# Optimization experiments

Hardware: AMD Instinct MI355X
Metric: run time of the kernel (lower is better)

## Reference

```python
import jax, jax.numpy as jnp
import numpy as np

NUM_STEPS = 8
N_ETYPES = 4
N_GRAPHS = 64


def setup_inputs() -> dict:
    key = jax.random.key(0)
    ks = jax.random.split(key, 16)
    N, E, D = 50000, 500000, 128
    features = jax.random.normal(ks[0], (N, D), dtype=jnp.float32)
    src = jax.random.randint(ks[1], (E,), 0, N, dtype=jnp.int32)
    dst = jax.random.randint(ks[2], (E,), 0, N, dtype=jnp.int32)
    edge_types = jax.random.randint(ks[3], (E,), 0, N_ETYPES, dtype=jnp.int32)
    graph_ids = jnp.sort(jax.random.randint(ks[4], (N,), 0, N_GRAPHS, dtype=jnp.int32))
    s = 1.0 / np.sqrt(D)
    # per-edge-type Linear(out,out): W[t] has shape [out,in], applied as x @ W.T + b
    W_etype = jax.random.uniform(ks[5], (N_ETYPES, D, D), jnp.float32, -s, s)
    b_etype = jax.random.uniform(ks[6], (N_ETYPES, D), jnp.float32, -s, s)
    # torch GRUCell(D, D) params
    W_ih = jax.random.uniform(ks[7], (3 * D, D), jnp.float32, -s, s)
    W_hh = jax.random.uniform(ks[8], (3 * D, D), jnp.float32, -s, s)
    b_ih = jax.random.uniform(ks[9], (3 * D,), jnp.float32, -s, s)
    b_hh = jax.random.uniform(ks[10], (3 * D,), jnp.float32, -s, s)
    cls_w = jax.random.uniform(ks[11], (1, D), jnp.float32, -s, s)
    cls_b = jax.random.uniform(ks[12], (1,), jnp.float32, -s, s)
    return dict(features=features, src=src, dst=dst, edge_types=edge_types,
                graph_ids=graph_ids, W_etype=W_etype, b_etype=b_etype,
                W_ih=W_ih, W_hh=W_hh, b_ih=b_ih, b_hh=b_hh,
                cls_w=cls_w, cls_b=cls_b)


def reference(features, src, dst, edge_types, graph_ids,
              W_etype, b_etype, W_ih, W_hh, b_ih, b_hh, cls_w, cls_b):
    N = features.shape[0]

    def step(h, _):
        # transform every node's state under every edge-type linear: [T, N, D]
        T = jnp.einsum('nd,tod->tno', h, W_etype) + b_etype[:, None, :]
        msg = T[edge_types, src]                      # [E, D] gather per edge
        a = jax.ops.segment_sum(msg, dst, num_segments=N)  # scatter-sum to dst
        # torch GRUCell
        gi = a @ W_ih.T + b_ih
        gh = h @ W_hh.T + b_hh
        i_r, i_z, i_n = jnp.split(gi, 3, axis=-1)
        h_r, h_z, h_n = jnp.split(gh, 3, axis=-1)
        r = jax.nn.sigmoid(i_r + h_r)
        z = jax.nn.sigmoid(i_z + h_z)
        n = jnp.tanh(i_n + r * h_n)
        h_new = (1.0 - z) * n + z * h
        return h_new, None

    h, _ = jax.lax.scan(step, features, None, length=NUM_STEPS)
    graph_sum = jax.ops.segment_sum(h, graph_ids, num_segments=N_GRAPHS)  # [B, D]
    logits = graph_sum @ cls_w.T + cls_b                                   # [B, 1]
    return jax.nn.sigmoid(logits).squeeze(-1)                              # [B]
```

## Files before the change

### kernel.cpp

```cpp
#include <hip/hip_runtime.h>

typedef __attribute__((ext_vector_type(4))) float floatx4;
typedef __attribute__((ext_vector_type(8))) _Float16 half8;

union H2 { unsigned int u; _Float16 h[2]; };

__device__ __forceinline__ float hs2f(unsigned short u) {
    union { unsigned short u; _Float16 h; } c; c.u = u; return (float)c.h;
}
__device__ __forceinline__ unsigned short f2hs(float f) {
    union { unsigned short u; _Float16 h; } c; c.h = (_Float16)f; return c.u;
}
__device__ __forceinline__ unsigned int pack2h(float a, float b) {
    H2 c; c.h[0] = (_Float16)a; c.h[1] = (_Float16)b; return c.u;
}

__device__ __forceinline__ void load_lds16(const unsigned short* g, unsigned short* l) {
    __builtin_amdgcn_global_load_lds(
        (__attribute__((address_space(1))) void*)(g),
        (__attribute__((address_space(3))) void*)(l), 16, 0, 0);
}

__global__ void k_hist(const int* __restrict__ dst, const int* __restrict__ et,
                       int* __restrict__ cnt4, int E) {
    int i = blockIdx.x * 256 + threadIdx.x;
    if (i < E) {
        atomicAdd(&cnt4[dst[i] * 4 + et[i]], 1);
    }
}

__global__ void k_scan_blk(const int* __restrict__ cnt4, int* __restrict__ row_ptr,
                           int* __restrict__ bsum, int N) {
    __shared__ int sm[256];
    int b = blockIdx.x, t = threadIdx.x, i = b * 256 + t;
    int v = 0;
    if (i < N) {
        const int4 q = ((const int4*)cnt4)[i];
        v = q.x + q.y + q.z + q.w;
    }
    sm[t] = v;
    __syncthreads();
    for (int off = 1; off < 256; off <<= 1) {
        int x = (t >= off) ? sm[t - off] : 0;
        __syncthreads();
        sm[t] += x;
        __syncthreads();
    }
    if (i < N) row_ptr[i] = sm[t] - v;
    if (t == 255) bsum[b] = sm[255];
}

__global__ void k_scan_top(int* __restrict__ bsum, int* __restrict__ boff,
                           int* __restrict__ row_ptr, int nblocks, int N) {
    __shared__ int sm[256];
    int t = threadIdx.x;
    int v = (t < nblocks) ? bsum[t] : 0;
    sm[t] = v;
    __syncthreads();
    for (int off = 1; off < 256; off <<= 1) {
        int x = (t >= off) ? sm[t - off] : 0;
        __syncthreads();
        sm[t] += x;
        __syncthreads();
    }
    if (t < nblocks) boff[t] = sm[t] - v;
    if (t == 255) row_ptr[N] = sm[255];
}

__global__ void k_scan_add(int* __restrict__ row_ptr, int* __restrict__ cursor4,
                           const int* __restrict__ boff, const int* __restrict__ cnt4, int N) {
    int i = blockIdx.x * 256 + threadIdx.x;
    if (i < N) {
        int r = row_ptr[i] + boff[blockIdx.x];
        row_ptr[i] = r;
        const int4 q = ((const int4*)cnt4)[i];
        int4 c;
        c.x = r;
        c.y = r + q.x;
        c.z = r + q.x + q.y;
        c.w = r + q.x + q.y + q.z;
        ((int4*)cursor4)[i] = c;
    }
}

__global__ void k_scatter(const int* __restrict__ src, const int* __restrict__ dst,
                          const int* __restrict__ et, int* __restrict__ cursor4,
                          int* __restrict__ edge_pk, int E) {
    int i = blockIdx.x * 256 + threadIdx.x;
    if (i < E) {
        int p = atomicAdd(&cursor4[dst[i] * 4 + et[i]], 1);
        edge_pk[p] = src[i];
    }
}

__global__ void k_init_h(const float* __restrict__ feat, unsigned short* __restrict__ AH, int N) {
    int i = blockIdx.x * 256 + threadIdx.x;
    if (i < N * 128) {
        int v = i >> 7, d = i & 127;
        AH[(size_t)v * 256 + 128 + d] = f2hs(feat[i]);
    }
}

__global__ void k_prep_wcat(const float* __restrict__ W, unsigned short* __restrict__ w) {
    int i = blockIdx.x * 256 + threadIdx.x;
    if (i < 65536) {
        int t = i >> 14, o = (i >> 7) & 127, d = i & 127;
        w[o * 512 + t * 128 + d] = f2hs(W[i]);
    }
}

__global__ void k_prep_wrz(const float* __restrict__ Wih, const float* __restrict__ Whh,
                           unsigned short* __restrict__ w) {
    int i = blockIdx.x * 256 + threadIdx.x;
    if (i < 256 * 256) {
        int j = i >> 8, k = i & 255;
        float v = (k < 128) ? Wih[j * 128 + k] : Whh[j * 128 + (k - 128)];
        w[i] = f2hs(v);
    }
}

__global__ void k_prep_wnh(const float* __restrict__ Wih, const float* __restrict__ Whh,
                           unsigned short* __restrict__ win, unsigned short* __restrict__ whn) {
    int i = blockIdx.x * 256 + threadIdx.x;
    if (i < 128 * 128) {
        int c = i >> 7, k = i & 127;
        win[i] = f2hs(Wih[(256 + c) * 128 + k]);
        whn[i] = f2hs(Whh[(256 + c) * 128 + k]);
    }
}

__global__ __launch_bounds__(256) void k_aggregate(
    const int* __restrict__ row_ptr, const int* __restrict__ cnt4,
    const int* __restrict__ edge_pk,
    const unsigned short* __restrict__ AH, unsigned short* __restrict__ S, int N)
{
    const int wv = threadIdx.x >> 6;
    const int lane = threadIdx.x & 63;
    const int v0 = blockIdx.x * 8 + wv * 2;
    if (v0 >= N) return;
    const int v1 = v0 + 1;
    const bool has1 = (v1 < N);

    const int beg0 = __builtin_amdgcn_readfirstlane(row_ptr[v0]);
    const int end0 = __builtin_amdgcn_readfirstlane(row_ptr[v0 + 1]);
    const int end1 = has1 ? __builtin_amdgcn_readfirstlane(row_ptr[v1 + 1]) : end0;
    const int4 q0 = ((const int4*)cnt4)[v0];
    const int c1 = beg0 + __builtin_amdgcn_readfirstlane(q0.x);
    const int c2 = c1 + __builtin_amdgcn_readfirstlane(q0.y);
    const int c3 = c2 + __builtin_amdgcn_readfirstlane(q0.z);
    const int c4 = end0;
    int c5 = end0, c6 = end0, c7 = end0;
    if (has1) {
        const int4 q1 = ((const int4*)cnt4)[v1];
        c5 = end0 + __builtin_amdgcn_readfirstlane(q1.x);
        c6 = c5 + __builtin_amdgcn_readfirstlane(q1.y);
        c7 = c6 + __builtin_amdgcn_readfirstlane(q1.z);
    }

    float a0x=0,a0y=0,a1x=0,a1y=0,a2x=0,a2y=0,a3x=0,a3y=0;
    float a4x=0,a4y=0,a5x=0,a5y=0,a6x=0,a6y=0,a7x=0,a7y=0;
    const unsigned short* hbase = AH + 128 + lane * 2;

    for (int e = beg0; e < end1; e += 12) {
        int sp[12];
        unsigned int hv[12];
#pragma unroll
        for (int u = 0; u < 12; ++u) {
            int idx = e + u;
            if (idx > end1 - 1) idx = end1 - 1;
            sp[u] = edge_pk[idx];
        }
#pragma unroll
        for (int u = 0; u < 12; ++u)
            hv[u] = *(const unsigned int*)(hbase + (size_t)sp[u] * 256);
#pragma unroll
        for (int u = 0; u < 12; ++u) {
            const int idx = e + u;
            if (idx < end1) {
                H2 c; c.u = hv[u];
                float x0 = (float)c.h[0];
                float x1 = (float)c.h[1];
                if (idx < c4) {
                    if (idx < c2) { if (idx < c1) { a0x+=x0; a0y+=x1; } else { a1x+=x0; a1y+=x1; } }
                    else          { if (idx < c3) { a2x+=x0; a2y+=x1; } else { a3x+=x0; a3y+=x1; } }
                } else {
                    if (idx < c6) { if (idx < c5) { a4x+=x0; a4y+=x1; } else { a5x+=x0; a5y+=x1; } }
                    else          { if (idx < c7) { a6x+=x0; a6y+=x1; } else { a7x+=x0; a7y+=x1; } }
                }
            }
        }
    }

    unsigned int* Sp0 = (unsigned int*)&S[(size_t)v0 * 512];
    Sp0[lane]       = pack2h(a0x, a0y);
    Sp0[64 + lane]  = pack2h(a1x, a1y);
    Sp0[128 + lane] = pack2h(a2x, a2y);
    Sp0[192 + lane] = pack2h(a3x, a3y);
    if (has1) {
        unsigned int* Sp1 = (unsigned int*)&S[(size_t)v1 * 512];
        Sp1[lane]       = pack2h(a4x, a4y);
        Sp1[64 + lane]  = pack2h(a5x, a5y);
        Sp1[128 + lane] = pack2h(a6x, a6y);
        Sp1[192 + lane] = pack2h(a7x, a7y);
    }
}

__global__ __launch_bounds__(256) void k_gemm0(
    const unsigned short* __restrict__ A, int M,
    const unsigned short* __restrict__ Bw,
    unsigned short* __restrict__ outAH, const int* __restrict__ cnt4,
    const float* __restrict__ b_et)
{
    __shared__ __align__(16) unsigned short As[2][64 * 32];
    __shared__ __align__(16) unsigned short Bs[2][128 * 32];
    const int tid  = threadIdx.x;
    const int lane = tid & 63;
    const int wv   = tid >> 6;
    const int wm   = (wv & 1) * 32;
    const int wn   = (wv >> 1) * 64;
    const int mBase = blockIdx.x * 64;
    const int srow = tid >> 2;
    const int sseg = (tid & 3) * 8;
    const int Ktot = 512;

    floatx4 acc[2][4];
#pragma unroll
    for (int i = 0; i < 2; ++i)
#pragma unroll
        for (int j = 0; j < 4; ++j) acc[i][j] = (floatx4){0.f, 0.f, 0.f, 0.f};

    int r0 = mBase + srow; if (r0 >= M) r0 = M - 1;

    for (int k0 = 0; k0 < Ktot; k0 += 64) {
        __syncthreads();
#pragma unroll
        for (int sub = 0; sub < 2; ++sub) {
            const int ko = k0 + sub * 32;
            load_lds16(A + (size_t)r0 * 512 + ko + sseg, &As[sub][srow * 32 + sseg]);
            const unsigned short* bw = Bw + (size_t)srow * Ktot + ko + sseg;
            load_lds16(bw,                     &Bs[sub][srow * 32 + sseg]);
            load_lds16(bw + (size_t)64 * Ktot, &Bs[sub][(srow + 64) * 32 + sseg]);
        }
        __syncthreads();
        const int kof = (lane >> 4) * 8;
        const int mr  = lane & 15;
#pragma unroll
        for (int p = 0; p < 2; ++p) {
            half8 af[2], bf[4];
#pragma unroll
            for (int i = 0; i < 2; ++i) af[i] = *(const half8*)&As[p][(wm + i * 16 + mr) * 32 + kof];
#pragma unroll
            for (int j = 0; j < 4; ++j) bf[j] = *(const half8*)&Bs[p][(wn + j * 16 + mr) * 32 + kof];
#pragma unroll
            for (int i = 0; i < 2; ++i)
#pragma unroll
                for (int j = 0; j < 4; ++j)
                    acc[i][j] = __builtin_amdgcn_mfma_f32_16x16x32_f16(af[i], bf[j], acc[i][j], 0, 0, 0);
        }
    }

    const int mr4 = (lane >> 4) * 4;
    const int nc  = lane & 15;
#pragma unroll
    for (int i = 0; i < 2; ++i) {
#pragma unroll
        for (int r = 0; r < 4; ++r) {
            int row = mBase + wm + i * 16 + mr4 + r;
            if (row < M) {
                int cx = cnt4[row * 4 + 0], cy = cnt4[row * 4 + 1];
                int cz = cnt4[row * 4 + 2], cw = cnt4[row * 4 + 3];
#pragma unroll
                for (int j = 0; j < 4; ++j) {
                    int col = wn + j * 16 + nc;
                    float val = acc[i][j][r]
                        + (float)cx * b_et[col]       + (float)cy * b_et[128 + col]
                        + (float)cz * b_et[256 + col] + (float)cw * b_et[384 + col];
                    outAH[(size_t)row * 256 + col] = f2hs(val);
                }
            }
        }
    }
}

__global__ __launch_bounds__(256) void k_gemm1(
    const unsigned short* __restrict__ A, int M,
    const unsigned short* __restrict__ Wrz,
    const unsigned short* __restrict__ Win, const unsigned short* __restrict__ Whn,
    _Float16* __restrict__ G)
{
    __shared__ __align__(16) unsigned short As[2][64 * 32];
    __shared__ __align__(16) unsigned short Bs[2][128 * 32];
    const int tid  = threadIdx.x;
    const int lane = tid & 63;
    const int wv   = tid >> 6;
    const int wm   = (wv & 1) * 32;
    const int wn   = (wv >> 1) * 64;
    const int mBase = blockIdx.x * 64;
    const int y    = blockIdx.y;
    const int srow = tid >> 2;
    const int sseg = (tid & 3) * 8;

    const unsigned short* Bw;
    int Ktot, aOff, colBase;
    if (y < 2)      { Bw = Wrz + (size_t)y * 128 * 256; Ktot = 256; aOff = 0;   colBase = y * 128; }
    else if (y == 2){ Bw = Win; Ktot = 128; aOff = 0;   colBase = 256; }
    else            { Bw = Whn; Ktot = 128; aOff = 128; colBase = 384; }

    floatx4 acc[2][4];
#pragma unroll
    for (int i = 0; i < 2; ++i)
#pragma unroll
        for (int j = 0; j < 4; ++j) acc[i][j] = (floatx4){0.f, 0.f, 0.f, 0.f};

    int r0 = mBase + srow; if (r0 >= M) r0 = M - 1;

    for (int k0 = 0; k0 < Ktot; k0 += 64) {
        __syncthreads();
#pragma unroll
        for (int sub = 0; sub < 2; ++sub) {
            const int ko = k0 + sub * 32;
            load_lds16(A + (size_t)r0 * 256 + aOff + ko + sseg, &As[sub][srow * 32 + sseg]);
            const unsigned short* bw = Bw + (size_t)srow * Ktot + ko + sseg;
            load_lds16(bw,                     &Bs[sub][srow * 32 + sseg]);
            load_lds16(bw + (size_t)64 * Ktot, &Bs[sub][(srow + 64) * 32 + sseg]);
        }
        __syncthreads();
        const int kof = (lane >> 4) * 8;
        const int mr  = lane & 15;
#pragma unroll
        for (int p = 0; p < 2; ++p) {
            half8 af[2], bf[4];
#pragma unroll
            for (int i = 0; i < 2; ++i) af[i] = *(const half8*)&As[p][(wm + i * 16 + mr) * 32 + kof];
#pragma unroll
            for (int j = 0; j < 4; ++j) bf[j] = *(const half8*)&Bs[p][(wn + j * 16 + mr) * 32 + kof];
#pragma unroll
            for (int i = 0; i < 2; ++i)
#pragma unroll
                for (int j = 0; j < 4; ++j)
                    acc[i][j] = __builtin_amdgcn_mfma_f32_16x16x32_f16(af[i], bf[j], acc[i][j], 0, 0, 0);
        }
    }

    const int mr4 = (lane >> 4) * 4;
    const int nc  = lane & 15;
#pragma unroll
    for (int i = 0; i < 2; ++i) {
#pragma unroll
        for (int r = 0; r < 4; ++r) {
            int row = mBase + wm + i * 16 + mr4 + r;
            if (row < M) {
#pragma unroll
                for (int j = 0; j < 4; ++j) {
                    int col = colBase + wn + j * 16 + nc;
                    G[(size_t)row * 512 + col] = (_Float16)acc[i][j][r];
                }
            }
        }
    }
}

__global__ void k_gru(const _Float16* __restrict__ G, unsigned short* __restrict__ AH,
                      const float* __restrict__ b_ih, const float* __restrict__ b_hh, int N) {
    int i = blockIdx.x * 256 + threadIdx.x;
    if (i >= N * 64) return;
    int v = i >> 6, j = i & 63;
    const unsigned int* g32 = (const unsigned int*)(G + (size_t)v * 512);
    H2 pr, pz, pn, ph;
    pr.u = g32[j];
    pz.u = g32[64 + j];
    pn.u = g32[128 + j];
    ph.u = g32[192 + j];
    H2 hv; hv.u = *(const unsigned int*)&AH[(size_t)v * 256 + 128 + j * 2];
    float outs[2];
#pragma unroll
    for (int q = 0; q < 2; ++q) {
        int d = j * 2 + q;
        float pre_r = (float)pr.h[q] + b_ih[d]       + b_hh[d];
        float pre_z = (float)pz.h[q] + b_ih[128 + d] + b_hh[128 + d];
        float i_n   = (float)pn.h[q] + b_ih[256 + d];
        float h_n   = (float)ph.h[q] + b_hh[256 + d];
        float r = 1.f / (1.f + __expf(-pre_r));
        float z = 1.f / (1.f + __expf(-pre_z));
        float n = tanhf(i_n + r * h_n);
        float h = (float)hv.h[q];
        outs[q] = (1.f - z) * n + z * h;
    }
    *(unsigned int*)&AH[(size_t)v * 256 + 128 + j * 2] = pack2h(outs[0], outs[1]);
}

__global__ void k_dotv(const unsigned short* __restrict__ AH, const float* __restrict__ cls_w,
                       float* __restrict__ dotv, int N) {
    int v = blockIdx.x * 4 + (threadIdx.x >> 6);
    int lane = threadIdx.x & 63;
    if (v >= N) return;
    H2 c; c.u = *(const unsigned int*)&AH[(size_t)v * 256 + 128 + lane * 2];
    float x = (float)c.h[0] * cls_w[lane * 2]
            + (float)c.h[1] * cls_w[lane * 2 + 1];
#pragma unroll
    for (int off = 32; off > 0; off >>= 1) x += __shfl_down(x, off);
    if (lane == 0) dotv[v] = x;
}

__global__ void k_gsum(const float* __restrict__ dotv, const int* __restrict__ gids,
                       const float* __restrict__ cls_b, float* __restrict__ out, int N) {
    int g = blockIdx.x;
    int t = threadIdx.x;
    int lo = 0, hi = N;
    while (lo < hi) { int m = (lo + hi) >> 1; if (gids[m] < g) lo = m + 1; else hi = m; }
    int s = lo;
    lo = 0; hi = N;
    while (lo < hi) { int m = (lo + hi) >> 1; if (gids[m] < g + 1) lo = m + 1; else hi = m; }
    int e = lo;
    float acc = 0.f;
    for (int v = s + t; v < e; v += 256) acc += dotv[v];
    __shared__ float red[256];
    red[t] = acc;
    __syncthreads();
    for (int off = 128; off > 0; off >>= 1) {
        if (t < off) red[t] += red[t + off];
        __syncthreads();
    }
    if (t == 0) out[g] = 1.f / (1.f + expf(-(red[0] + cls_b[0])));
}

extern "C" void kernel_launch(void* const* d_in, const int* in_sizes, int n_in,
                              void* d_out, int out_size, void* d_ws, size_t ws_size,
                              hipStream_t stream) {
    const float* features = (const float*)d_in[0];
    const int*   src      = (const int*)d_in[1];
    const int*   dst      = (const int*)d_in[2];
    const int*   etype    = (const int*)d_in[3];
    const int*   gids     = (const int*)d_in[4];
    const float* W_etype  = (const float*)d_in[5];
    const float* b_etype  = (const float*)d_in[6];
    const float* W_ih     = (const float*)d_in[7];
    const float* W_hh     = (const float*)d_in[8];
    const float* b_ih     = (const float*)d_in[9];
    const float* b_hh     = (const float*)d_in[10];
    const float* cls_w    = (const float*)d_in[11];
    const float* cls_b    = (const float*)d_in[12];
    const int N = in_sizes[0] / 128;
    const int E = in_sizes[1];
    float* out = (float*)d_out;

    char* ws = (char*)d_ws;
    size_t off = 0;
    auto alloc = [&](size_t bytes) -> void* {
        off = (off + 255) & ~(size_t)255;
        void* p = ws + off;
        off += bytes;
        return p;
    };
    unsigned short* AH  = (unsigned short*)alloc((size_t)N * 256 * 2);
    unsigned short* S   = (unsigned short*)alloc((size_t)N * 512 * 2);
    _Float16*       G   = (_Float16*)alloc((size_t)N * 512 * 2);
    unsigned short* Wc  = (unsigned short*)alloc(128 * 512 * 2);
    unsigned short* Wrz = (unsigned short*)alloc(256 * 256 * 2);
    unsigned short* Win = (unsigned short*)alloc(128 * 128 * 2);
    unsigned short* Whn = (unsigned short*)alloc(128 * 128 * 2);
    int* row_ptr = (int*)alloc((size_t)(N + 1) * 4);
    int* cursor4 = (int*)alloc((size_t)N * 16);
    int* cnt4    = (int*)alloc((size_t)N * 16);
    int* edge_pk = (int*)alloc((size_t)E * 4);
    float* dotv  = (float*)alloc((size_t)N * 4);
    int* bsum    = (int*)alloc(256 * 4);
    int* boff    = (int*)alloc(256 * 4);
    (void)ws_size; (void)n_in;

    const int nscan = (N + 255) / 256;
    hipMemsetAsync(cnt4, 0, (size_t)N * 16, stream);
    k_hist<<<(E + 255) / 256, 256, 0, stream>>>(dst, etype, cnt4, E);
    k_scan_blk<<<nscan, 256, 0, stream>>>(cnt4, row_ptr, bsum, N);
    k_scan_top<<<1, 256, 0, stream>>>(bsum, boff, row_ptr, nscan, N);
    k_scan_add<<<nscan, 256, 0, stream>>>(row_ptr, cursor4, boff, cnt4, N);
    k_scatter<<<(E + 255) / 256, 256, 0, stream>>>(src, dst, etype, cursor4, edge_pk, E);
    k_init_h<<<(N * 128 + 255) / 256, 256, 0, stream>>>(features, AH, N);
    k_prep_wcat<<<65536 / 256, 256, 0, stream>>>(W_etype, Wc);
    k_prep_wrz<<<(256 * 256) / 256, 256, 0, stream>>>(W_ih, W_hh, Wrz);
    k_prep_wnh<<<(128 * 128) / 256, 256, 0, stream>>>(W_ih, W_hh, Win, Whn);

    const int mblocks64 = (N + 63) / 64;
    for (int s = 0; s < 8; ++s) {
        k_aggregate<<<(N + 7) / 8, 256, 0, stream>>>(row_ptr, cnt4, edge_pk, AH, S, N);
        k_gemm0<<<mblocks64, 256, 0, stream>>>(S, N, Wc, AH, cnt4, b_etype);
        dim3 g2(mblocks64, 4);
        k_gemm1<<<g2, 256, 0, stream>>>(AH, N, Wrz, Win, Whn, G);
        k_gru<<<(N * 64 + 255) / 256, 256, 0, stream>>>(G, AH, b_ih, b_hh, N);
    }
    k_dotv<<<(N + 3) / 4, 256, 0, stream>>>(AH, cls_w, dotv, N);
    k_gsum<<<out_size, 256, 0, stream>>>(dotv, gids, cls_b, out, N);
}
```

Baseline: 958.4 us.

## Fuse GRU gate GEMMs and elementwise update into one kernel

Replaces the 4-way split gate GEMM plus a separate GRU elementwise kernel with a single kernel per 64-row tile. It computes the r/z, i_n and h_n products in sequence and applies the GRU update in the epilogue, writing h back into AH in place. This removes the N×512 fp16 G buffer round trip and one launch per step. In exchange the grid has a quarter as many blocks, register pressure is higher (r, z and n results are kept packed in registers), and the per-element epilogue stores are strided. The in-place write is safe only because each block reads just its own rows.

```diff
diff --git a/kernel.cpp b/kernel.cpp
--- a/kernel.cpp
+++ b/kernel.cpp
@@ -282,51 +282,95 @@
     }
 }
 
-__global__ __launch_bounds__(256) void k_gemm1(
-    const unsigned short* __restrict__ A, int M,
+__global__ __launch_bounds__(256) void k_gates(
+    unsigned short* AH, int M,
     const unsigned short* __restrict__ Wrz,
     const unsigned short* __restrict__ Win, const unsigned short* __restrict__ Whn,
-    _Float16* __restrict__ G)
+    const float* __restrict__ b_ih, const float* __restrict__ b_hh)
 {
     __shared__ __align__(16) unsigned short As[2][64 * 32];
-    __shared__ __align__(16) unsigned short Bs[2][128 * 32];
+    __shared__ __align__(16) unsigned short Bs[2][256 * 32];
     const int tid  = threadIdx.x;
     const int lane = tid & 63;
     const int wv   = tid >> 6;
     const int wm   = (wv & 1) * 32;
     const int wn   = (wv >> 1) * 64;
     const int mBase = blockIdx.x * 64;
-    const int y    = blockIdx.y;
     const int srow = tid >> 2;
     const int sseg = (tid & 3) * 8;
-
-    const unsigned short* Bw;
-    int Ktot, aOff, colBase;
-    if (y < 2)      { Bw = Wrz + (size_t)y * 128 * 256; Ktot = 256; aOff = 0;   colBase = y * 128; }
-    else if (y == 2){ Bw = Win; Ktot = 128; aOff = 0;   colBase = 256; }
-    else            { Bw = Whn; Ktot = 128; aOff = 128; colBase = 384; }
-
-    floatx4 acc[2][4];
+    const int kof  = (lane >> 4) * 8;
+    const int mr   = lane & 15;
+
+    int r0 = mBase + srow; if (r0 >= M) r0 = M - 1;
+
+    floatx4 acc_r[2][4], acc_z[2][4];
 #pragma unroll
     for (int i = 0; i < 2; ++i)
 #pragma unroll
-        for (int j = 0; j < 4; ++j) acc[i][j] = (floatx4){0.f, 0.f, 0.f, 0.f};
-
-    int r0 = mBase + srow; if (r0 >= M) r0 = M - 1;
-
-    for (int k0 = 0; k0 < Ktot; k0 += 64) {
+        for (int j = 0; j < 4; ++j) {
+            acc_r[i][j] = (floatx4){0.f, 0.f, 0.f, 0.f};
+            acc_z[i][j] = (floatx4){0.f, 0.f, 0.f, 0.f};
+        }
+
+    for (int k0 = 0; k0 < 256; k0 += 64) {
         __syncthreads();
 #pragma unroll
         for (int sub = 0; sub < 2; ++sub) {
             const int ko = k0 + sub * 32;
-            load_lds16(A + (size_t)r0 * 256 + aOff + ko + sseg, &As[sub][srow * 32 + sseg]);
-            const unsigned short* bw = Bw + (size_t)srow * Ktot + ko + sseg;
-            load_lds16(bw,                     &Bs[sub][srow * 32 + sseg]);
-            load_lds16(bw + (size_t)64 * Ktot, &Bs[sub][(srow + 64) * 32 + sseg]);
-        }
-        __syncthreads();
-        const int kof = (lane >> 4) * 8;
-        const int mr  = lane & 15;
+            load_lds16(AH + (size_t)r0 * 256 + ko + sseg, &As[sub][srow * 32 + sseg]);
+            const unsigned short* b = Wrz + (size_t)srow * 256 + ko + sseg;
+            load_lds16(b,                     &Bs[sub][srow * 32 + sseg]);
+            load_lds16(b + (size_t)64 * 256,  &Bs[sub][(srow + 64) * 32 + sseg]);
+            load_lds16(b + (size_t)128 * 256, &Bs[sub][(srow + 128) * 32 + sseg]);
+            load_lds16(b + (size_t)192 * 256, &Bs[sub][(srow + 192) * 32 + sseg]);
+        }
+        __syncthreads();
+#pragma unroll
+        for (int p = 0; p < 2; ++p) {
+            half8 af[2], br[4], bz[4];
+#pragma unroll
+            for (int i = 0; i < 2; ++i) af[i] = *(const half8*)&As[p][(wm + i * 16 + mr) * 32 + kof];
+#pragma unroll
+            for (int j = 0; j < 4; ++j) br[j] = *(const half8*)&Bs[p][(wn + j * 16 + mr) * 32 + kof];
+#pragma unroll
+            for (int j = 0; j < 4; ++j) bz[j] = *(const half8*)&Bs[p][(128 + wn + j * 16 + mr) * 32 + kof];
+#pragma unroll
+            for (int i = 0; i < 2; ++i)
+#pragma unroll
+                for (int j = 0; j < 4; ++j) {
+                    acc_r[i][j] = __builtin_amdgcn_mfma_f32_16x16x32_f16(af[i], br[j], acc_r[i][j], 0, 0, 0);
+                    acc_z[i][j] = __builtin_amdgcn_mfma_f32_16x16x32_f16(af[i], bz[j], acc_z[i][j], 0, 0, 0);
+                }
+        }
+    }
+    unsigned int r_pk[2][4][2], z_pk[2][4][2];
+#pragma unroll
+    for (int i = 0; i < 2; ++i)
+#pragma unroll
+        for (int j = 0; j < 4; ++j) {
+            r_pk[i][j][0] = pack2h(acc_r[i][j][0], acc_r[i][j][1]);
+            r_pk[i][j][1] = pack2h(acc_r[i][j][2], acc_r[i][j][3]);
+            z_pk[i][j][0] = pack2h(acc_z[i][j][0], acc_z[i][j][1]);
+            z_pk[i][j][1] = pack2h(acc_z[i][j][2], acc_z[i][j][3]);
+        }
+
+    floatx4 acc_n[2][4];
+#pragma unroll
+    for (int i = 0; i < 2; ++i)
+#pragma unroll
+        for (int j = 0; j < 4; ++j) acc_n[i][j] = (floatx4){0.f, 0.f, 0.f, 0.f};
+
+    for (int k0 = 0; k0 < 128; k0 += 64) {
+        __syncthreads();
+#pragma unroll
+        for (int sub = 0; sub < 2; ++sub) {
+            const int ko = k0 + sub * 32;
+            load_lds16(AH + (size_t)r0 * 256 + ko + sseg, &As[sub][srow * 32 + sseg]);
+            const unsigned short* b = Win + (size_t)srow * 128 + ko + sseg;
+            load_lds16(b,                    &Bs[sub][srow * 32 + sseg]);
+            load_lds16(b + (size_t)64 * 128, &Bs[sub][(srow + 64) * 32 + sseg]);
+        }
+        __syncthreads();
 #pragma unroll
         for (int p = 0; p < 2; ++p) {
             half8 af[2], bf[4];
@@ -338,55 +382,82 @@
             for (int i = 0; i < 2; ++i)
 #pragma unroll
                 for (int j = 0; j < 4; ++j)
-                    acc[i][j] = __builtin_amdgcn_mfma_f32_16x16x32_f16(af[i], bf[j], acc[i][j], 0, 0, 0);
+                    acc_n[i][j] = __builtin_amdgcn_mfma_f32_16x16x32_f16(af[i], bf[j], acc_n[i][j], 0, 0, 0);
+        }
+    }
+    unsigned int n_pk[2][4][2];
+#pragma unroll
+    for (int i = 0; i < 2; ++i)
+#pragma unroll
+        for (int j = 0; j < 4; ++j) {
+            n_pk[i][j][0] = pack2h(acc_n[i][j][0], acc_n[i][j][1]);
+            n_pk[i][j][1] = pack2h(acc_n[i][j][2], acc_n[i][j][3]);
+        }
+
+    floatx4 acc_h[2][4];
+#pragma unroll
+    for (int i = 0; i < 2; ++i)
+#pragma unroll
+        for (int j = 0; j < 4; ++j) acc_h[i][j] = (floatx4){0.f, 0.f, 0.f, 0.f};
+
+    for (int k0 = 0; k0 < 128; k0 += 64) {
+        __syncthreads();
+#pragma unroll
+        for (int sub = 0; sub < 2; ++sub) {
+            const int ko = k0 + sub * 32;
+            load_lds16(AH + (size_t)r0 * 256 + 128 + ko + sseg, &As[sub][srow * 32 + sseg]);
+            const unsigned short* b = Whn + (size_t)srow * 128 + ko + sseg;
+            load_lds16(b,                    &Bs[sub][srow * 32 + sseg]);
+            load_lds16(b + (size_t)64 * 128, &Bs[sub][(srow + 64) * 32 + sseg]);
+        }
+        __syncthreads();
+#pragma unroll
+        for (int p = 0; p < 2; ++p) {
+            half8 af[2], bf[4];
+#pragma unroll
+            for (int i = 0; i < 2; ++i) af[i] = *(const half8*)&As[p][(wm + i * 16 + mr) * 32 + kof];
+#pragma unroll
+            for (int j = 0; j < 4; ++j) bf[j] = *(const half8*)&Bs[p][(wn + j * 16 + mr) * 32 + kof];
+#pragma unroll
+            for (int i = 0; i < 2; ++i)
+#pragma unroll
+                for (int j = 0; j < 4; ++j)
+                    acc_h[i][j] = __builtin_amdgcn_mfma_f32_16x16x32_f16(af[i], bf[j], acc_h[i][j], 0, 0, 0);
         }
     }
 
     const int mr4 = (lane >> 4) * 4;
     const int nc  = lane & 15;
 #pragma unroll
-    for (int i = 0; i < 2; ++i) {
-#pragma unroll
-        for (int r = 0; r < 4; ++r) {
-            int row = mBase + wm + i * 16 + mr4 + r;
-            if (row < M) {
-#pragma unroll
-                for (int j = 0; j < 4; ++j) {
-                    int col = colBase + wn + j * 16 + nc;
-                    G[(size_t)row * 512 + col] = (_Float16)acc[i][j][r];
+    for (int j = 0; j < 4; ++j) {
+        const int col = wn + j * 16 + nc;
+        const float b_r  = b_ih[col]       + b_hh[col];
+        const float b_z  = b_ih[128 + col] + b_hh[128 + col];
+        const float b_in = b_ih[256 + col];
+        const float b_hn = b_hh[256 + col];
+#pragma unroll
+        for (int i = 0; i < 2; ++i) {
+#pragma unroll
+            for (int r = 0; r < 4; ++r) {
+                int row = mBase + wm + i * 16 + mr4 + r;
+                if (row < M) {
+                    H2 cr; cr.u = r_pk[i][j][r >> 1];
+                    H2 cz; cz.u = z_pk[i][j][r >> 1];
+                    H2 cn; cn.u = n_pk[i][j][r >> 1];
+                    float rv = (float)cr.h[r & 1] + b_r;
+                    float zv = (float)cz.h[r & 1] + b_z;
+                    float iv = (float)cn.h[r & 1] + b_in;
+                    float hv = acc_h[i][j][r] + b_hn;
+                    rv = 1.f / (1.f + __expf(-rv));
+                    zv = 1.f / (1.f + __expf(-zv));
+                    float nv = tanhf(iv + rv * hv);
+                    size_t off = (size_t)row * 256 + 128 + col;
+                    float h = hs2f(AH[off]);
+                    AH[off] = f2hs((1.f - zv) * nv + zv * h);
                 }
             }
         }
     }
-}
-
-__global__ void k_gru(const _Float16* __restrict__ G, unsigned short* __restrict__ AH,
-                      const float* __restrict__ b_ih, const float* __restrict__ b_hh, int N) {
-    int i = blockIdx.x * 256 + threadIdx.x;
-    if (i >= N * 64) return;
-    int v = i >> 6, j = i & 63;
-    const unsigned int* g32 = (const unsigned int*)(G + (size_t)v * 512);
-    H2 pr, pz, pn, ph;
-    pr.u = g32[j];
-    pz.u = g32[64 + j];
-    pn.u = g32[128 + j];
-    ph.u = g32[192 + j];
-    H2 hv; hv.u = *(const unsigned int*)&AH[(size_t)v * 256 + 128 + j * 2];
-    float outs[2];
-#pragma unroll
-    for (int q = 0; q < 2; ++q) {
-        int d = j * 2 + q;
-        float pre_r = (float)pr.h[q] + b_ih[d]       + b_hh[d];
-        float pre_z = (float)pz.h[q] + b_ih[128 + d] + b_hh[128 + d];
-        float i_n   = (float)pn.h[q] + b_ih[256 + d];
-        float h_n   = (float)ph.h[q] + b_hh[256 + d];
-        float r = 1.f / (1.f + __expf(-pre_r));
-        float z = 1.f / (1.f + __expf(-pre_z));
-        float n = tanhf(i_n + r * h_n);
-        float h = (float)hv.h[q];
-        outs[q] = (1.f - z) * n + z * h;
-    }
-    *(unsigned int*)&AH[(size_t)v * 256 + 128 + j * 2] = pack2h(outs[0], outs[1]);
 }
 
 __global__ void k_dotv(const unsigned short* __restrict__ AH, const float* __restrict__ cls_w,
@@ -454,7 +525,6 @@
     };
     unsigned short* AH  = (unsigned short*)alloc((size_t)N * 256 * 2);
     unsigned short* S   = (unsigned short*)alloc((size_t)N * 512 * 2);
-    _Float16*       G   = (_Float16*)alloc((size_t)N * 512 * 2);
     unsigned short* Wc  = (unsigned short*)alloc(128 * 512 * 2);
     unsigned short* Wrz = (unsigned short*)alloc(256 * 256 * 2);
     unsigned short* Win = (unsigned short*)alloc(128 * 128 * 2);
@@ -484,9 +554,7 @@
     for (int s = 0; s < 8; ++s) {
         k_aggregate<<<(N + 7) / 8, 256, 0, stream>>>(row_ptr, cnt4, edge_pk, AH, S, N);
         k_gemm0<<<mblocks64, 256, 0, stream>>>(S, N, Wc, AH, cnt4, b_etype);
-        dim3 g2(mblocks64, 4);
-        k_gemm1<<<g2, 256, 0, stream>>>(AH, N, Wrz, Win, Whn, G);
-        k_gru<<<(N * 64 + 255) / 256, 256, 0, stream>>>(G, AH, b_ih, b_hh, N);
+        k_gates<<<mblocks64, 256, 0, stream>>>(AH, N, Wrz, Win, Whn, b_ih, b_hh);
     }
     k_dotv<<<(N + 3) / 4, 256, 0, stream>>>(AH, cls_w, dotv, N);
     k_gsum<<<out_size, 256, 0, stream>>>(dotv, gids, cls_b, out, N);
```

Measured after the change: 1.241 ms. 1.3x slower.

## Transform node states per edge type before gathering instead of aggregating first

Applied to the files above, without the earlier changes.

Reorders the message step: a GEMM first computes T[t] = h @ W_t for all four edge types into a [4N,128] buffer, then the aggregate kernel gathers T rows indexed by a packed (type*N+src) edge id and adds count-weighted biases. This removes the per-destination 4-way type split and the wide [N,512] intermediate S along with its K=512 GEMM. In exchange the GEMM writes a 4N×128 half buffer and the gather reads 256-byte rows, so the total gather volume is about the same.

```diff
diff --git a/kernel.cpp b/kernel.cpp
--- a/kernel.cpp
+++ b/kernel.cpp
@@ -85,11 +85,11 @@
 
 __global__ void k_scatter(const int* __restrict__ src, const int* __restrict__ dst,
                           const int* __restrict__ et, int* __restrict__ cursor4,
-                          int* __restrict__ edge_pk, int E) {
+                          int* __restrict__ edge_pk, int E, int Nn) {
     int i = blockIdx.x * 256 + threadIdx.x;
     if (i < E) {
         int p = atomicAdd(&cursor4[dst[i] * 4 + et[i]], 1);
-        edge_pk[p] = src[i];
+        edge_pk[p] = et[i] * Nn + src[i];
     }
 }
 
@@ -101,12 +101,9 @@
     }
 }
 
-__global__ void k_prep_wcat(const float* __restrict__ W, unsigned short* __restrict__ w) {
-    int i = blockIdx.x * 256 + threadIdx.x;
-    if (i < 65536) {
-        int t = i >> 14, o = (i >> 7) & 127, d = i & 127;
-        w[o * 512 + t * 128 + d] = f2hs(W[i]);
-    }
+__global__ void k_prep_wc2(const float* __restrict__ W, unsigned short* __restrict__ w) {
+    int i = blockIdx.x * 256 + threadIdx.x;
+    if (i < 65536) w[i] = f2hs(W[i]);
 }
 
 __global__ void k_prep_wrz(const float* __restrict__ Wih, const float* __restrict__ Whh,
@@ -129,87 +126,10 @@
     }
 }
 
-__global__ __launch_bounds__(256) void k_aggregate(
-    const int* __restrict__ row_ptr, const int* __restrict__ cnt4,
-    const int* __restrict__ edge_pk,
-    const unsigned short* __restrict__ AH, unsigned short* __restrict__ S, int N)
-{
-    const int wv = threadIdx.x >> 6;
-    const int lane = threadIdx.x & 63;
-    const int v0 = blockIdx.x * 8 + wv * 2;
-    if (v0 >= N) return;
-    const int v1 = v0 + 1;
-    const bool has1 = (v1 < N);
-
-    const int beg0 = __builtin_amdgcn_readfirstlane(row_ptr[v0]);
-    const int end0 = __builtin_amdgcn_readfirstlane(row_ptr[v0 + 1]);
-    const int end1 = has1 ? __builtin_amdgcn_readfirstlane(row_ptr[v1 + 1]) : end0;
-    const int4 q0 = ((const int4*)cnt4)[v0];
-    const int c1 = beg0 + __builtin_amdgcn_readfirstlane(q0.x);
-    const int c2 = c1 + __builtin_amdgcn_readfirstlane(q0.y);
-    const int c3 = c2 + __builtin_amdgcn_readfirstlane(q0.z);
-    const int c4 = end0;
-    int c5 = end0, c6 = end0, c7 = end0;
-    if (has1) {
-        const int4 q1 = ((const int4*)cnt4)[v1];
-        c5 = end0 + __builtin_amdgcn_readfirstlane(q1.x);
-        c6 = c5 + __builtin_amdgcn_readfirstlane(q1.y);
-        c7 = c6 + __builtin_amdgcn_readfirstlane(q1.z);
-    }
-
-    float a0x=0,a0y=0,a1x=0,a1y=0,a2x=0,a2y=0,a3x=0,a3y=0;
-    float a4x=0,a4y=0,a5x=0,a5y=0,a6x=0,a6y=0,a7x=0,a7y=0;
-    const unsigned short* hbase = AH + 128 + lane * 2;
-
-    for (int e = beg0; e < end1; e += 12) {
-        int sp[12];
-        unsigned int hv[12];
-#pragma unroll
-        for (int u = 0; u < 12; ++u) {
-            int idx = e + u;
-            if (idx > end1 - 1) idx = end1 - 1;
-            sp[u] = edge_pk[idx];
-        }
-#pragma unroll
-        for (int u = 0; u < 12; ++u)
-            hv[u] = *(const unsigned int*)(hbase + (size_t)sp[u] * 256);
-#pragma unroll
-        for (int u = 0; u < 12; ++u) {
-            const int idx = e + u;
-            if (idx < end1) {
-                H2 c; c.u = hv[u];
-                float x0 = (float)c.h[0];
-                float x1 = (float)c.h[1];
-                if (idx < c4) {
-                    if (idx < c2) { if (idx < c1) { a0x+=x0; a0y+=x1; } else { a1x+=x0; a1y+=x1; } }
-                    else          { if (idx < c3) { a2x+=x0; a2y+=x1; } else { a3x+=x0; a3y+=x1; } }
-                } else {
-                    if (idx < c6) { if (idx < c5) { a4x+=x0; a4y+=x1; } else { a5x+=x0; a5y+=x1; } }
-                    else          { if (idx < c7) { a6x+=x0; a6y+=x1; } else { a7x+=x0; a7y+=x1; } }
-                }
-            }
-        }
-    }
-
-    unsigned int* Sp0 = (unsigned int*)&S[(size_t)v0 * 512];
-    Sp0[lane]       = pack2h(a0x, a0y);
-    Sp0[64 + lane]  = pack2h(a1x, a1y);
-    Sp0[128 + lane] = pack2h(a2x, a2y);
-    Sp0[192 + lane] = pack2h(a3x, a3y);
-    if (has1) {
-        unsigned int* Sp1 = (unsigned int*)&S[(size_t)v1 * 512];
-        Sp1[lane]       = pack2h(a4x, a4y);
-        Sp1[64 + lane]  = pack2h(a5x, a5y);
-        Sp1[128 + lane] = pack2h(a6x, a6y);
-        Sp1[192 + lane] = pack2h(a7x, a7y);
-    }
-}
-
-__global__ __launch_bounds__(256) void k_gemm0(
-    const unsigned short* __restrict__ A, int M,
-    const unsigned short* __restrict__ Bw,
-    unsigned short* __restrict__ outAH, const int* __restrict__ cnt4,
-    const float* __restrict__ b_et)
+__global__ __launch_bounds__(256) void k_gemm_pre(
+    const unsigned short* __restrict__ AH, int M, int Nn,
+    const unsigned short* __restrict__ Wc2,
+    unsigned short* __restrict__ T)
 {
     __shared__ __align__(16) unsigned short As[2][64 * 32];
     __shared__ __align__(16) unsigned short Bs[2][128 * 32];
@@ -219,9 +139,11 @@
     const int wm   = (wv & 1) * 32;
     const int wn   = (wv >> 1) * 64;
     const int mBase = blockIdx.x * 64;
+    const int y    = blockIdx.y;
     const int srow = tid >> 2;
     const int sseg = (tid & 3) * 8;
-    const int Ktot = 512;
+    const int Ktot = 128;
+    const unsigned short* Bw = Wc2 + (size_t)y * 128 * 128;
 
     floatx4 acc[2][4];
 #pragma unroll
@@ -236,7 +158,7 @@
 #pragma unroll
         for (int sub = 0; sub < 2; ++sub) {
             const int ko = k0 + sub * 32;
-            load_lds16(A + (size_t)r0 * 512 + ko + sseg, &As[sub][srow * 32 + sseg]);
+            load_lds16(AH + (size_t)r0 * 256 + 128 + ko + sseg, &As[sub][srow * 32 + sseg]);
             const unsigned short* bw = Bw + (size_t)srow * Ktot + ko + sseg;
             load_lds16(bw,                     &Bs[sub][srow * 32 + sseg]);
             load_lds16(bw + (size_t)64 * Ktot, &Bs[sub][(srow + 64) * 32 + sseg]);
@@ -267,18 +189,76 @@
         for (int r = 0; r < 4; ++r) {
             int row = mBase + wm + i * 16 + mr4 + r;
             if (row < M) {
-                int cx = cnt4[row * 4 + 0], cy = cnt4[row * 4 + 1];
-                int cz = cnt4[row * 4 + 2], cw = cnt4[row * 4 + 3];
 #pragma unroll
                 for (int j = 0; j < 4; ++j) {
                     int col = wn + j * 16 + nc;
-                    float val = acc[i][j][r]
-                        + (float)cx * b_et[col]       + (float)cy * b_et[128 + col]
-                        + (float)cz * b_et[256 + col] + (float)cw * b_et[384 + col];
-                    outAH[(size_t)row * 256 + col] = f2hs(val);
+                    T[((size_t)y * Nn + row) * 128 + col] = f2hs(acc[i][j][r]);
                 }
             }
         }
+    }
+}
+
+__global__ __launch_bounds__(256) void k_aggregate2(
+    const int* __restrict__ row_ptr, const int* __restrict__ cnt4,
+    const int* __restrict__ edge_pk,
+    const unsigned short* __restrict__ T, const float* __restrict__ b_et,
+    unsigned short* __restrict__ AH, int N)
+{
+    const int wv = threadIdx.x >> 6;
+    const int lane = threadIdx.x & 63;
+    const int v0 = blockIdx.x * 8 + wv * 2;
+    if (v0 >= N) return;
+    const int v1 = v0 + 1;
+    const bool has1 = (v1 < N);
+
+    const int beg0 = __builtin_amdgcn_readfirstlane(row_ptr[v0]);
+    const int end0 = __builtin_amdgcn_readfirstlane(row_ptr[v0 + 1]);
+    const int end1 = has1 ? __builtin_amdgcn_readfirstlane(row_ptr[v1 + 1]) : end0;
+
+    float a0x = 0, a0y = 0, a1x = 0, a1y = 0;
+    const unsigned short* tbase = T + lane * 2;
+
+    for (int e = beg0; e < end1; e += 12) {
+        int sp[12];
+        unsigned int hv[12];
+#pragma unroll
+        for (int u = 0; u < 12; ++u) {
+            int idx = e + u;
+            if (idx > end1 - 1) idx = end1 - 1;
+            sp[u] = edge_pk[idx];
+        }
+#pragma unroll
+        for (int u = 0; u < 12; ++u)
+            hv[u] = *(const unsigned int*)(tbase + (size_t)sp[u] * 128);
+#pragma unroll
+        for (int u = 0; u < 12; ++u) {
+            const int idx = e + u;
+            if (idx < end1) {
+                H2 c; c.u = hv[u];
+                float x0 = (float)c.h[0];
+                float x1 = (float)c.h[1];
+                if (idx < end0) { a0x += x0; a0y += x1; }
+                else            { a1x += x0; a1y += x1; }
+            }
+        }
+    }
+
+    const float2 b0 = *(const float2*)&b_et[0 * 128 + lane * 2];
+    const float2 b1 = *(const float2*)&b_et[1 * 128 + lane * 2];
+    const float2 b2 = *(const float2*)&b_et[2 * 128 + lane * 2];
+    const float2 b3 = *(const float2*)&b_et[3 * 128 + lane * 2];
+    {
+        const int4 q = ((const int4*)cnt4)[v0];
+        float bx = (float)q.x * b0.x + (float)q.y * b1.x + (float)q.z * b2.x + (float)q.w * b3.x;
+        float by = (float)q.x * b0.y + (float)q.y * b1.y + (float)q.z * b2.y + (float)q.w * b3.y;
+        *(unsigned int*)&AH[(size_t)v0 * 256 + lane * 2] = pack2h(a0x + bx, a0y + by);
+    }
+    if (has1) {
+        const int4 q = ((const int4*)cnt4)[v1];
+        float bx = (float)q.x * b0.x + (float)q.y * b1.x + (float)q.z * b2.x + (float)q.w * b3.x;
+        float by = (float)q.x * b0.y + (float)q.y * b1.y + (float)q.z * b2.y + (float)q.w * b3.y;
+        *(unsigned int*)&AH[(size_t)v1 * 256 + lane * 2] = pack2h(a1x + bx, a1y + by);
     }
 }
 
@@ -453,9 +433,9 @@
         return p;
     };
     unsigned short* AH  = (unsigned short*)alloc((size_t)N * 256 * 2);
-    unsigned short* S   = (unsigned short*)alloc((size_t)N * 512 * 2);
+    unsigned short* T   = (unsigned short*)alloc((size_t)4 * N * 128 * 2);
     _Float16*       G   = (_Float16*)alloc((size_t)N * 512 * 2);
-    unsigned short* Wc  = (unsigned short*)alloc(128 * 512 * 2);
+    unsigned short* Wc2 = (unsigned short*)alloc(4 * 128 * 128 * 2);
     unsigned short* Wrz = (unsigned short*)alloc(256 * 256 * 2);
     unsigned short* Win = (unsigned short*)alloc(128 * 128 * 2);
     unsigned short* Whn = (unsigned short*)alloc(128 * 128 * 2);
@@ -474,16 +454,17 @@
     k_scan_blk<<<nscan, 256, 0, stream>>>(cnt4, row_ptr, bsum, N);
     k_scan_top<<<1, 256, 0, stream>>>(bsum, boff, row_ptr, nscan, N);
     k_scan_add<<<nscan, 256, 0, stream>>>(row_ptr, cursor4, boff, cnt4, N);
-    k_scatter<<<(E + 255) / 256, 256, 0, stream>>>(src, dst, etype, cursor4, edge_pk, E);
+    k_scatter<<<(E + 255) / 256, 256, 0, stream>>>(src, dst, etype, cursor4, edge_pk, E, N);
     k_init_h<<<(N * 128 + 255) / 256, 256, 0, stream>>>(features, AH, N);
-    k_prep_wcat<<<65536 / 256, 256, 0, stream>>>(W_etype, Wc);
+    k_prep_wc2<<<65536 / 256, 256, 0, stream>>>(W_etype, Wc2);
     k_prep_wrz<<<(256 * 256) / 256, 256, 0, stream>>>(W_ih, W_hh, Wrz);
     k_prep_wnh<<<(128 * 128) / 256, 256, 0, stream>>>(W_ih, W_hh, Win, Whn);
 
     const int mblocks64 = (N + 63) / 64;
     for (int s = 0; s < 8; ++s) {
-        k_aggregate<<<(N + 7) / 8, 256, 0, stream>>>(row_ptr, cnt4, edge_pk, AH, S, N);
-        k_gemm0<<<mblocks64, 256, 0, stream>>>(S, N, Wc, AH, cnt4, b_etype);
+        dim3 gp(mblocks64, 4);
+        k_gemm_pre<<<gp, 256, 0, stream>>>(AH, N, N, Wc2, T);
+        k_aggregate2<<<(N + 7) / 8, 256, 0, stream>>>(row_ptr, cnt4, edge_pk, T, b_etype, AH, N);
         dim3 g2(mblocks64, 4);
         k_gemm1<<<g2, 256, 0, stream>>>(AH, N, Wrz, Win, Whn, G);
         k_gru<<<(N * 64 + 255) / 256, 256, 0, stream>>>(G, AH, b_ih, b_hh, N);
```

Measured after the change: 942.5 us. About the same (-1.7%).
